# Kernel optimization log

Hardware: AMD Instinct MI355X
Metric: run time of the kernel (lower is better)

Reference implementation:

```python
import jax, jax.numpy as jnp
import numpy as np

N_NODES = 100000
N_EDGES = 1000000
NODE_DIM = 128
LR_VOCAB = 2000
LR_EMBED = 32
HIDDEN = 128
IN_DIM = NODE_DIM * 4 + 1 + LR_EMBED  # 545


def setup_inputs() -> dict:
    key = jax.random.key(0)
    ks = jax.random.split(key, 10)
    z = jax.random.normal(ks[0], (N_NODES, NODE_DIM), dtype=jnp.float32)
    edge_index = jax.random.randint(ks[1], (2, N_EDGES), 0, N_NODES, dtype=jnp.int64)
    # edge_attr7: col 0 = dist (float in [0,1)), col 2 = lr_id (int-valued float in [0, LR_VOCAB))
    ea = jax.random.uniform(ks[2], (N_EDGES, 7), dtype=jnp.float32)
    lr_ids = jax.random.randint(ks[3], (N_EDGES,), 0, LR_VOCAB).astype(jnp.float32)
    edge_attr7 = ea.at[:, 2].set(lr_ids)
    lr_emb = jax.random.normal(ks[4], (LR_VOCAB, LR_EMBED), dtype=jnp.float32) * 0.02
    W1 = jax.random.normal(ks[5], (IN_DIM, HIDDEN), dtype=jnp.float32) * 0.02
    b1 = jnp.zeros((HIDDEN,), dtype=jnp.float32)
    W2 = jax.random.normal(ks[6], (HIDDEN, HIDDEN), dtype=jnp.float32) * 0.02
    b2 = jnp.zeros((HIDDEN,), dtype=jnp.float32)
    W3 = jax.random.normal(ks[7], (HIDDEN, 1), dtype=jnp.float32) * 0.02
    b3 = jnp.zeros((1,), dtype=jnp.float32)
    return {"z": z, "edge_index": edge_index, "edge_attr7": edge_attr7,
            "lr_emb": lr_emb, "W1": W1, "b1": b1, "W2": W2, "b2": b2,
            "W3": W3, "b3": b3}


def reference(z, edge_index, edge_attr7, lr_emb, W1, b1, W2, b2, W3, b3):
    src = edge_index[0]
    dst = edge_index[1]
    zs = z[src]                      # [E, D]
    zd = z[dst]                      # [E, D]
    dist = edge_attr7[:, 0:1]        # [E, 1]
    lr_id = edge_attr7[:, 2].astype(jnp.int32)
    lr_vec = lr_emb[lr_id]           # [E, LR_EMBED]
    x = jnp.concatenate([zs, zd, zs * zd, jnp.abs(zs - zd), dist, lr_vec], axis=1)  # [E, IN_DIM]
    h = jax.nn.relu(x @ W1 + b1)     # dropout is identity at inference
    h = jax.nn.relu(h @ W2 + b2)
    logit = (h @ W3 + b3).reshape(-1)  # [E]
    return logit
```

## Files before the change

kernel.cpp:

```cpp
#include <hip/hip_runtime.h>

#define N_EDGES 1000000
#define HID 128
#define ME 64
#define CW 136

typedef unsigned short ushort;
typedef unsigned int uint;
typedef __attribute__((ext_vector_type(8))) short short8;
typedef __attribute__((ext_vector_type(4))) float f32x4;

__device__ __forceinline__ float blo(uint u) { return __builtin_bit_cast(float, u << 16); }
__device__ __forceinline__ float bhi(uint u) { return __builtin_bit_cast(float, u & 0xffff0000u); }
__device__ __forceinline__ ushort f2bfbits(float f) {
  uint u = __builtin_bit_cast(uint, f);
  return (ushort)((u + 0x7fffu + ((u >> 16) & 1u)) >> 16);
}
__device__ __forceinline__ uint cvtpk(float a, float b) {
  uint r;
  asm("v_cvt_pk_bf16_f32 %0, %1, %2" : "=v"(r) : "v"(a), "v"(b));
  return r;
}

__global__ void prep_kernel(const float* __restrict__ W1, const float* __restrict__ W2,
                            ushort* __restrict__ W1p, ushort* __restrict__ W2p) {
  const int t = blockIdx.x * blockDim.x + threadIdx.x;
  const int n1 = 18 * 8 * 64 * 8;
  if (t < n1) {
    const int j = t & 7, lane = (t >> 3) & 63, nt = (t >> 9) & 7, kb = t >> 12;
    const int col = nt * 16 + (lane & 15);
    float val = 0.f;
    if (kb < 16) {
      const int k = kb * 32 + (lane >> 4) * 8 + j;
      val = W1[k * HID + col];
    } else {
      const int c = (kb - 16) * 32 + (lane >> 4) * 8 + j;
      const int k = (c == 0) ? 512 : ((c >= 2 && c < 34) ? (511 + c) : -1);
      if (k >= 0) val = W1[k * HID + col];
    }
    W1p[t] = f2bfbits(val);
  } else {
    const int t2 = t - n1;
    if (t2 < 4 * 8 * 64 * 8) {
      const int j = t2 & 7, lane = (t2 >> 3) & 63, nt = (t2 >> 9) & 7, kb = t2 >> 12;
      const int k = kb * 32 + (lane >> 4) * 8 + j;
      const int col = nt * 16 + (lane & 15);
      W2p[t2] = f2bfbits(W2[k * HID + col]);
    }
  }
}

__global__ __launch_bounds__(256, 4)
void edge_mlp(const float* __restrict__ z, const int* __restrict__ ei,
              const float* __restrict__ ea, const float* __restrict__ lre,
              const ushort* __restrict__ W1p, const float* __restrict__ b1,
              const ushort* __restrict__ W2p, const float* __restrict__ b2,
              const float* __restrict__ W3, const float* __restrict__ b3,
              float* __restrict__ out) {
  __shared__ ushort B0[ME][CW];
  __shared__ ushort B1[ME][CW];

  const int tid = threadIdx.x;
  const int lane = tid & 63;
  const int w = tid >> 6;
  const int r15 = lane & 15;
  const int g = lane >> 4;
  const int half = lane >> 5;
  const int li = lane & 31;
  const int row0 = w * 16;
  const int cw = w * 32;
  const int eb = blockIdx.x * ME;

  int sd = 0;
  float auxv = 0.f;
  if (lane < 16)      sd = ei[eb + row0 + lane];
  else if (lane < 32) sd = ei[N_EDGES + eb + row0 + (lane - 16)];
  else if (lane < 48) auxv = ea[(eb + row0 + (lane - 32)) * 7 + 0];
  else                auxv = ea[(eb + row0 + (lane - 48)) * 7 + 2];

  float4 vs[8], vd[8];
#pragma unroll
  for (int t = 0; t < 8; ++t) {
    const int e = 2 * t + half;
    const int s = __shfl(sd, e);
    vs[t] = *(const float4*)(z + s * HID + 4 * li);
  }
#pragma unroll
  for (int t = 0; t < 8; ++t) {
    const int e = 2 * t + half;
    const int d = __shfl(sd, 16 + e);
    vd[t] = *(const float4*)(z + d * HID + 4 * li);
  }
  uint2 zs_pk[8], zd_pk[8];
#pragma unroll
  for (int t = 0; t < 8; ++t) {
    zs_pk[t].x = cvtpk(vs[t].x, vs[t].y);
    zs_pk[t].y = cvtpk(vs[t].z, vs[t].w);
    zd_pk[t].x = cvtpk(vd[t].x, vd[t].y);
    zd_pk[t].y = cvtpk(vd[t].z, vd[t].w);
  }
#pragma unroll
  for (int t = 0; t < 8; ++t) {
    const int r = row0 + 2 * t + half;
    *(uint2*)&B0[r][4 * li] = zs_pk[t];
    *(uint2*)&B1[r][4 * li] = zd_pk[t];
  }
  __syncthreads();

  f32x4 acc[4][2];
#pragma unroll
  for (int mt = 0; mt < 4; ++mt) {
    acc[mt][0] = (f32x4){0.f, 0.f, 0.f, 0.f};
    acc[mt][1] = (f32x4){0.f, 0.f, 0.f, 0.f};
  }

#define MFMA_CHUNK(BUF, NKK, KB)                                                        \
  _Pragma("unroll")                                                                     \
  for (int kk = 0; kk < (NKK); ++kk) {                                                  \
    const int kbg = (KB) + kk;                                                          \
    short8 bfr0 = *(const short8*)(W1p + (((kbg * 8 + 2 * w) * 64) + lane) * 8);        \
    short8 bfr1 = *(const short8*)(W1p + (((kbg * 8 + 2 * w + 1) * 64) + lane) * 8);    \
    _Pragma("unroll")                                                                   \
    for (int mt = 0; mt < 4; ++mt) {                                                    \
      short8 af = *(const short8*)&BUF[mt * 16 + r15][kk * 32 + g * 8];                 \
      acc[mt][0] = __builtin_amdgcn_mfma_f32_16x16x32_bf16(af, bfr0, acc[mt][0], 0, 0, 0); \
      acc[mt][1] = __builtin_amdgcn_mfma_f32_16x16x32_bf16(af, bfr1, acc[mt][1], 0, 0, 0); \
    }                                                                                   \
  }

  MFMA_CHUNK(B0, 4, 0)
  __syncthreads();

#pragma unroll
  for (int t = 0; t < 8; ++t) {
    const int r = row0 + 2 * t + half;
    uint2 o;
    o.x = cvtpk(blo(zs_pk[t].x) * blo(zd_pk[t].x), bhi(zs_pk[t].x) * bhi(zd_pk[t].x));
    o.y = cvtpk(blo(zs_pk[t].y) * blo(zd_pk[t].y), bhi(zs_pk[t].y) * bhi(zd_pk[t].y));
    *(uint2*)&B0[r][4 * li] = o;
  }
  MFMA_CHUNK(B1, 4, 4)
  __syncthreads();

#pragma unroll
  for (int t = 0; t < 8; ++t) {
    const int r = row0 + 2 * t + half;
    uint2 o;
    o.x = cvtpk(fabsf(blo(zs_pk[t].x) - blo(zd_pk[t].x)),
                fabsf(bhi(zs_pk[t].x) - bhi(zd_pk[t].x)));
    o.y = cvtpk(fabsf(blo(zs_pk[t].y) - blo(zd_pk[t].y)),
                fabsf(bhi(zs_pk[t].y) - bhi(zd_pk[t].y)));
    *(uint2*)&B1[r][4 * li] = o;
  }
  MFMA_CHUNK(B0, 4, 8)
  __syncthreads();

  {
    const float dv = __shfl(auxv, 32 + r15);
    if (lane < 16) B0[row0 + lane][0] = f2bfbits(dv);
  }
#pragma unroll
  for (int t = 0; t < 4; ++t) {
    const int e = 4 * t + g;
    const int lrid = (int)__shfl(auxv, 48 + e);
    const float2 lv = *(const float2*)(lre + lrid * 32 + 2 * r15);
    *(uint*)&B0[row0 + e][2 + 2 * r15] = cvtpk(lv.x, lv.y);
  }
  MFMA_CHUNK(B1, 4, 12)
  __syncthreads();

  MFMA_CHUNK(B0, 2, 16)
  {
    const float b1v0 = b1[cw + r15];
    const float b1v1 = b1[cw + 16 + r15];
#pragma unroll
    for (int mt = 0; mt < 4; ++mt)
#pragma unroll
      for (int nt = 0; nt < 2; ++nt)
#pragma unroll
        for (int j = 0; j < 4; ++j) {
          const float h = acc[mt][nt][j] + (nt ? b1v1 : b1v0);
          B1[mt * 16 + g * 4 + j][cw + nt * 16 + r15] = f2bfbits(fmaxf(h, 0.f));
        }
  }
  __syncthreads();

  f32x4 acc2[4][2];
#pragma unroll
  for (int mt = 0; mt < 4; ++mt) {
    acc2[mt][0] = (f32x4){0.f, 0.f, 0.f, 0.f};
    acc2[mt][1] = (f32x4){0.f, 0.f, 0.f, 0.f};
  }
#pragma unroll
  for (int kk = 0; kk < 4; ++kk) {
    short8 bfr0 = *(const short8*)(W2p + (((kk * 8 + 2 * w) * 64) + lane) * 8);
    short8 bfr1 = *(const short8*)(W2p + (((kk * 8 + 2 * w + 1) * 64) + lane) * 8);
#pragma unroll
    for (int mt = 0; mt < 4; ++mt) {
      short8 af = *(const short8*)&B1[mt * 16 + r15][kk * 32 + g * 8];
      acc2[mt][0] = __builtin_amdgcn_mfma_f32_16x16x32_bf16(af, bfr0, acc2[mt][0], 0, 0, 0);
      acc2[mt][1] = __builtin_amdgcn_mfma_f32_16x16x32_bf16(af, bfr1, acc2[mt][1], 0, 0, 0);
    }
  }
  {
    const float b2v0 = b2[cw + r15];
    const float b2v1 = b2[cw + 16 + r15];
#pragma unroll
    for (int mt = 0; mt < 4; ++mt)
#pragma unroll
      for (int nt = 0; nt < 2; ++nt)
#pragma unroll
        for (int j = 0; j < 4; ++j) {
          const float h = acc2[mt][nt][j] + (nt ? b2v1 : b2v0);
          B0[mt * 16 + g * 4 + j][cw + nt * 16 + r15] = f2bfbits(fmaxf(h, 0.f));
        }
  }
  __syncthreads();

  {
    const int rr = w * 16 + r15;
    float sum = 0.f;
#pragma unroll
    for (int i = 0; i < 4; ++i) {
      const int c0 = g * 32 + i * 8;
      const uint4 hv = *(const uint4*)&B0[rr][c0];
#pragma unroll
      for (int p = 0; p < 4; ++p) {
        const uint u = ((const uint*)&hv)[p];
        const float2 wv = *(const float2*)(W3 + c0 + 2 * p);
        sum += blo(u) * wv.x + bhi(u) * wv.y;
      }
    }
    sum += __shfl_xor(sum, 16);
    sum += __shfl_xor(sum, 32);
    if (lane < 16) out[eb + rr] = sum + b3[0];
  }
}

extern "C" void kernel_launch(void* const* d_in, const int* in_sizes, int n_in,
                              void* d_out, int out_size, void* d_ws, size_t ws_size,
                              hipStream_t stream) {
  const float* z   = (const float*)d_in[0];
  const int*   ei  = (const int*)d_in[1];
  const float* ea  = (const float*)d_in[2];
  const float* lre = (const float*)d_in[3];
  const float* W1  = (const float*)d_in[4];
  const float* b1  = (const float*)d_in[5];
  const float* W2  = (const float*)d_in[6];
  const float* b2  = (const float*)d_in[7];
  const float* W3  = (const float*)d_in[8];
  const float* b3  = (const float*)d_in[9];
  float* out = (float*)d_out;

  ushort* W1p = (ushort*)d_ws;
  ushort* W2p = W1p + 18 * 8 * 64 * 8;

  prep_kernel<<<352, 256, 0, stream>>>(W1, W2, W1p, W2p);
  edge_mlp<<<N_EDGES / ME, 256, 0, stream>>>(z, ei, ea, lre, W1p, b1, W2p, b2, W3, b3, out);
}
```

Before: 301.1 us.

## Swap padded LDS rows for XOR-swizzled layout and raise occupancy hint

Replaces the padded 136-wide shared tiles with unpadded 128-wide tiles addressed through an XOR swizzle of the column by row, which cuts LDS per block and is meant to avoid bank conflicts. The launch bound rises from 4 to 5 blocks per CU, and the z gather loops are restructured to convert each load to bf16 right away, shrinking live registers. The risk is register spilling under the tighter bound and less memory-level parallelism in the gather, since loads are no longer all issued before the conversions.

```diff
diff --git a/kernel.cpp b/kernel.cpp
--- a/kernel.cpp
+++ b/kernel.cpp
@@ -3,7 +3,6 @@
 #define N_EDGES 1000000
 #define HID 128
 #define ME 64
-#define CW 136
 
 typedef unsigned short ushort;
 typedef unsigned int uint;
@@ -20,6 +19,9 @@
   uint r;
   asm("v_cvt_pk_bf16_f32 %0, %1, %2" : "=v"(r) : "v"(a), "v"(b));
   return r;
+}
+__device__ __forceinline__ int sidx(int r, int c) {
+  return r * 128 + (c ^ ((r & 7) << 3));
 }
 
 __global__ void prep_kernel(const float* __restrict__ W1, const float* __restrict__ W2,
@@ -50,15 +52,15 @@
   }
 }
 
-__global__ __launch_bounds__(256, 4)
+__global__ __launch_bounds__(256, 5)
 void edge_mlp(const float* __restrict__ z, const int* __restrict__ ei,
               const float* __restrict__ ea, const float* __restrict__ lre,
               const ushort* __restrict__ W1p, const float* __restrict__ b1,
               const ushort* __restrict__ W2p, const float* __restrict__ b2,
               const float* __restrict__ W3, const float* __restrict__ b3,
               float* __restrict__ out) {
-  __shared__ ushort B0[ME][CW];
-  __shared__ ushort B1[ME][CW];
+  __shared__ ushort B0[ME * 128];
+  __shared__ ushort B1[ME * 128];
 
   const int tid = threadIdx.x;
   const int lane = tid & 63;
@@ -78,32 +80,26 @@
   else if (lane < 48) auxv = ea[(eb + row0 + (lane - 32)) * 7 + 0];
   else                auxv = ea[(eb + row0 + (lane - 48)) * 7 + 2];
 
-  float4 vs[8], vd[8];
-#pragma unroll
-  for (int t = 0; t < 8; ++t) {
-    const int e = 2 * t + half;
-    const int s = __shfl(sd, e);
-    vs[t] = *(const float4*)(z + s * HID + 4 * li);
-  }
-#pragma unroll
-  for (int t = 0; t < 8; ++t) {
-    const int e = 2 * t + half;
-    const int d = __shfl(sd, 16 + e);
-    vd[t] = *(const float4*)(z + d * HID + 4 * li);
-  }
   uint2 zs_pk[8], zd_pk[8];
 #pragma unroll
   for (int t = 0; t < 8; ++t) {
-    zs_pk[t].x = cvtpk(vs[t].x, vs[t].y);
-    zs_pk[t].y = cvtpk(vs[t].z, vs[t].w);
-    zd_pk[t].x = cvtpk(vd[t].x, vd[t].y);
-    zd_pk[t].y = cvtpk(vd[t].z, vd[t].w);
+    const int s = __shfl(sd, 2 * t + half);
+    const float4 v = *(const float4*)(z + s * HID + 4 * li);
+    zs_pk[t].x = cvtpk(v.x, v.y);
+    zs_pk[t].y = cvtpk(v.z, v.w);
+  }
+#pragma unroll
+  for (int t = 0; t < 8; ++t) {
+    const int d = __shfl(sd, 16 + 2 * t + half);
+    const float4 v = *(const float4*)(z + d * HID + 4 * li);
+    zd_pk[t].x = cvtpk(v.x, v.y);
+    zd_pk[t].y = cvtpk(v.z, v.w);
   }
 #pragma unroll
   for (int t = 0; t < 8; ++t) {
     const int r = row0 + 2 * t + half;
-    *(uint2*)&B0[r][4 * li] = zs_pk[t];
-    *(uint2*)&B1[r][4 * li] = zd_pk[t];
+    *(uint2*)&B0[sidx(r, 4 * li)] = zs_pk[t];
+    *(uint2*)&B1[sidx(r, 4 * li)] = zd_pk[t];
   }
   __syncthreads();
 
@@ -122,7 +118,7 @@
     short8 bfr1 = *(const short8*)(W1p + (((kbg * 8 + 2 * w + 1) * 64) + lane) * 8);    \
     _Pragma("unroll")                                                                   \
     for (int mt = 0; mt < 4; ++mt) {                                                    \
-      short8 af = *(const short8*)&BUF[mt * 16 + r15][kk * 32 + g * 8];                 \
+      short8 af = *(const short8*)&BUF[sidx(mt * 16 + r15, kk * 32 + g * 8)];           \
       acc[mt][0] = __builtin_amdgcn_mfma_f32_16x16x32_bf16(af, bfr0, acc[mt][0], 0, 0, 0); \
       acc[mt][1] = __builtin_amdgcn_mfma_f32_16x16x32_bf16(af, bfr1, acc[mt][1], 0, 0, 0); \
     }                                                                                   \
@@ -137,7 +133,7 @@
     uint2 o;
     o.x = cvtpk(blo(zs_pk[t].x) * blo(zd_pk[t].x), bhi(zs_pk[t].x) * bhi(zd_pk[t].x));
     o.y = cvtpk(blo(zs_pk[t].y) * blo(zd_pk[t].y), bhi(zs_pk[t].y) * bhi(zd_pk[t].y));
-    *(uint2*)&B0[r][4 * li] = o;
+    *(uint2*)&B0[sidx(r, 4 * li)] = o;
   }
   MFMA_CHUNK(B1, 4, 4)
   __syncthreads();
@@ -150,21 +146,21 @@
                 fabsf(bhi(zs_pk[t].x) - bhi(zd_pk[t].x)));
     o.y = cvtpk(fabsf(blo(zs_pk[t].y) - blo(zd_pk[t].y)),
                 fabsf(bhi(zs_pk[t].y) - bhi(zd_pk[t].y)));
-    *(uint2*)&B1[r][4 * li] = o;
+    *(uint2*)&B1[sidx(r, 4 * li)] = o;
   }
   MFMA_CHUNK(B0, 4, 8)
   __syncthreads();
 
   {
     const float dv = __shfl(auxv, 32 + r15);
-    if (lane < 16) B0[row0 + lane][0] = f2bfbits(dv);
+    if (lane < 16) B0[sidx(row0 + lane, 0)] = f2bfbits(dv);
   }
 #pragma unroll
   for (int t = 0; t < 4; ++t) {
     const int e = 4 * t + g;
     const int lrid = (int)__shfl(auxv, 48 + e);
     const float2 lv = *(const float2*)(lre + lrid * 32 + 2 * r15);
-    *(uint*)&B0[row0 + e][2 + 2 * r15] = cvtpk(lv.x, lv.y);
+    *(uint*)&B0[sidx(row0 + e, 2 + 2 * r15)] = cvtpk(lv.x, lv.y);
   }
   MFMA_CHUNK(B1, 4, 12)
   __syncthreads();
@@ -180,7 +176,7 @@
 #pragma unroll
         for (int j = 0; j < 4; ++j) {
           const float h = acc[mt][nt][j] + (nt ? b1v1 : b1v0);
-          B1[mt * 16 + g * 4 + j][cw + nt * 16 + r15] = f2bfbits(fmaxf(h, 0.f));
+          B1[sidx(mt * 16 + g * 4 + j, cw + nt * 16 + r15)] = f2bfbits(fmaxf(h, 0.f));
         }
   }
   __syncthreads();
@@ -197,7 +193,7 @@
     short8 bfr1 = *(const short8*)(W2p + (((kk * 8 + 2 * w + 1) * 64) + lane) * 8);
 #pragma unroll
     for (int mt = 0; mt < 4; ++mt) {
-      short8 af = *(const short8*)&B1[mt * 16 + r15][kk * 32 + g * 8];
+      short8 af = *(const short8*)&B1[sidx(mt * 16 + r15, kk * 32 + g * 8)];
       acc2[mt][0] = __builtin_amdgcn_mfma_f32_16x16x32_bf16(af, bfr0, acc2[mt][0], 0, 0, 0);
       acc2[mt][1] = __builtin_amdgcn_mfma_f32_16x16x32_bf16(af, bfr1, acc2[mt][1], 0, 0, 0);
     }
@@ -212,7 +208,7 @@
 #pragma unroll
         for (int j = 0; j < 4; ++j) {
           const float h = acc2[mt][nt][j] + (nt ? b2v1 : b2v0);
-          B0[mt * 16 + g * 4 + j][cw + nt * 16 + r15] = f2bfbits(fmaxf(h, 0.f));
+          B0[sidx(mt * 16 + g * 4 + j, cw + nt * 16 + r15)] = f2bfbits(fmaxf(h, 0.f));
         }
   }
   __syncthreads();
@@ -223,7 +219,7 @@
 #pragma unroll
     for (int i = 0; i < 4; ++i) {
       const int c0 = g * 32 + i * 8;
-      const uint4 hv = *(const uint4*)&B0[rr][c0];
+      const uint4 hv = *(const uint4*)&B0[sidx(rr, c0)];
 #pragma unroll
       for (int p = 0; p < 4; ++p) {
         const uint u = ((const uint*)&hv)[p];
```

Result: slower. 525.2 us (+74.4%).
